# Optimization experiments

Hardware: AMD Instinct MI355X
Metric: run time of the kernel (lower is better)

The kernel has to match this reference:

```python
import jax, jax.numpy as jnp
import numpy as np

EMB_DIM = 1024
N_HEAD = 16
HEAD_SIZE = 64
B = 2
T = 2048


def setup_inputs() -> dict:
    key = jax.random.key(0)
    k_x, k_qkv, k_pw, k_pb = jax.random.split(key, 4)
    x = jax.random.normal(k_x, (B, T, EMB_DIM), dtype=jnp.float32)
    # nn.Linear(emb_dim, 3*emb_dim, bias=False): y = x @ W_qkv, W_qkv: [C, 3C]
    W_qkv = jax.random.normal(k_qkv, (EMB_DIM, 3 * EMB_DIM), dtype=jnp.float32) * (EMB_DIM ** -0.5)
    # nn.Linear(emb_dim, emb_dim) with bias
    W_proj = jax.random.normal(k_pw, (EMB_DIM, EMB_DIM), dtype=jnp.float32) * (EMB_DIM ** -0.5)
    b_proj = jax.random.normal(k_pb, (EMB_DIM,), dtype=jnp.float32) * 0.01
    return {"x": x, "W_qkv": W_qkv, "W_proj": W_proj, "b_proj": b_proj}


def reference(x, W_qkv, W_proj, b_proj):
    Bn, Tn, C = x.shape
    qkv = x @ W_qkv                          # [B, T, 3C]
    q, k, v = jnp.split(qkv, 3, axis=-1)
    # [B, T, H, D] -> attention over heads via einsum (no explicit transpose)
    q = q.reshape(Bn, Tn, N_HEAD, HEAD_SIZE)
    k = k.reshape(Bn, Tn, N_HEAD, HEAD_SIZE)
    v = v.reshape(Bn, Tn, N_HEAD, HEAD_SIZE)
    att = jnp.einsum("bthd,bshd->bhts", q, k) * (HEAD_SIZE ** -0.5)  # [B, H, T, T]
    causal = jnp.tril(jnp.ones((Tn, Tn), dtype=bool))
    att = jnp.where(causal, att, -jnp.inf)
    att = jax.nn.softmax(att, axis=-1)
    y = jnp.einsum("bhts,bshd->bthd", att, v).reshape(Bn, Tn, C)
    return y @ W_proj + b_proj
```

## Files before the change

kernel.cpp:

```cpp
#include <hip/hip_runtime.h>
#include <hip/hip_bf16.h>

typedef unsigned short u16;
typedef unsigned int u32;
typedef u16 u16x4 __attribute__((ext_vector_type(4)));
typedef u16 u16x8 __attribute__((ext_vector_type(8)));
typedef u32 u32x4 __attribute__((ext_vector_type(4)));
typedef __bf16 bf16x8 __attribute__((ext_vector_type(8)));
typedef float f32x4 __attribute__((ext_vector_type(4)));

__device__ __forceinline__ u16 f2bf(float f) {
  union { float f; unsigned u; } v; v.f = f;
  unsigned r = v.u + 0x7fffu + ((v.u >> 16) & 1u);
  return (u16)(r >> 16);
}

__device__ __forceinline__ u16 bf(float f) {
  __bf16 h = (__bf16)f;
  union { __bf16 h; u16 u; } c; c.h = h;
  return c.u;
}

__device__ __forceinline__ u32 pack2(float lo, float hi) {
  return (u32)bf(lo) | ((u32)bf(hi) << 16);
}

__device__ __forceinline__ float fexp2(float x) {
#if __has_builtin(__builtin_amdgcn_exp2f)
  return __builtin_amdgcn_exp2f(x);
#else
  return exp2f(x);
#endif
}

__device__ __forceinline__ float frcp(float x) {
#if __has_builtin(__builtin_amdgcn_rcpf)
  return __builtin_amdgcn_rcpf(x);
#else
  return 1.0f / x;
#endif
}

__device__ __forceinline__ void gload16(const void* g, void* l) {
  __builtin_amdgcn_global_load_lds((const __attribute__((address_space(1))) void*)g,
                                   (__attribute__((address_space(3))) void*)l, 16, 0, 0);
}

__global__ __launch_bounds__(256) void cvt_bf16(const float* __restrict__ in,
                                                u16* __restrict__ out, int n) {
  int i = (blockIdx.x * 256 + threadIdx.x) * 8;
  if (i >= n) return;
  f32x4 a = *(const f32x4*)(in + i);
  f32x4 b = *(const f32x4*)(in + i + 4);
  u16x8 r;
  r[0] = f2bf(a[0]); r[1] = f2bf(a[1]); r[2] = f2bf(a[2]); r[3] = f2bf(a[3]);
  r[4] = f2bf(b[0]); r[5] = f2bf(b[1]); r[6] = f2bf(b[2]); r[7] = f2bf(b[3]);
  *(u16x8*)(out + i) = r;
}

__global__ __launch_bounds__(256) void transpose_w(
    const float* __restrict__ Wqkv, const float* __restrict__ Wproj,
    u16* __restrict__ wqT, u16* __restrict__ wpT)
{
  __shared__ float tile[32][33];
  int bx = blockIdx.x;
  const float* in;
  u16* out;
  int N;
  if (bx < 96) { in = Wqkv; out = wqT; N = 3072; }
  else         { in = Wproj; out = wpT; N = 1024; bx -= 96; }
  const int K = 1024;
  int n0 = bx * 32, k0 = blockIdx.y * 32;
  int tx = threadIdx.x & 31, ty = threadIdx.x >> 5;
  for (int i = 0; i < 32; i += 8)
    tile[ty + i][tx] = in[(long)(k0 + ty + i) * N + n0 + tx];
  __syncthreads();
  for (int i = 0; i < 32; i += 8)
    out[(long)(n0 + ty + i) * K + k0 + tx] = f2bf(tile[tx][ty + i]);
}

template<int BM, int BN, bool F32OUT>
__global__ __launch_bounds__(256) void gemm_bt(
    const u16* __restrict__ A, const u16* __restrict__ Bt,
    void* __restrict__ Cp, const float* __restrict__ bias,
    int M, int N, int K)
{
  constexpr int MR = BM / 32, NR = BN / 32;
  constexpr int RA = BM / 32, RB = BN / 32;
  __shared__ char lds[(BM + BN) * 128];
  char* As = lds;
  char* Bs = lds + BM * 128;
  const int tid = threadIdx.x;
  const int l = tid & 63, w = tid >> 6;
  const int wr = w >> 1, wc = w & 1;
  const int lr = l & 15, q4 = l >> 4;
  const long row0 = (long)blockIdx.x * BM;
  const long col0 = (long)blockIdx.y * BN;

  f32x4 acc[MR][NR] = {};

  const u16* gA[RA];
  int oA[RA];
  for (int i = 0; i < RA; ++i) {
    int cc = i * 256 + tid;
    int r = cc >> 3, c = (cc & 7) ^ (r & 7);
    oA[i] = cc * 16;
    gA[i] = A + (row0 + r) * K + c * 8;
  }
  const u16* gB[RB];
  int oB[RB];
  for (int i = 0; i < RB; ++i) {
    int cc = i * 256 + tid;
    int r = cc >> 3, c = (cc & 7) ^ (r & 7);
    oB[i] = cc * 16;
    gB[i] = Bt + (col0 + r) * K + c * 8;
  }

  for (int k0 = 0; k0 < K; k0 += 64) {
    __syncthreads();
    for (int i = 0; i < RA; ++i) gload16(gA[i] + k0, As + oA[i]);
    for (int i = 0; i < RB; ++i) gload16(gB[i] + k0, Bs + oB[i]);
    __syncthreads();
    for (int kk = 0; kk < 2; ++kk) {
      bf16x8 a[MR], b[NR];
      for (int m = 0; m < MR; ++m) {
        int r = wr * (BM / 2) + m * 16 + lr;
        a[m] = *(const bf16x8*)(As + r * 128 + (((kk * 4 + q4) ^ (r & 7)) << 4));
      }
      for (int n = 0; n < NR; ++n) {
        int r = wc * (BN / 2) + n * 16 + lr;
        b[n] = *(const bf16x8*)(Bs + r * 128 + (((kk * 4 + q4) ^ (r & 7)) << 4));
      }
      for (int m = 0; m < MR; ++m)
        for (int n = 0; n < NR; ++n)
          acc[m][n] = __builtin_amdgcn_mfma_f32_16x16x32_bf16(a[m], b[n], acc[m][n], 0, 0, 0);
    }
  }

  for (int n = 0; n < NR; ++n) {
    int col = (int)col0 + wc * (BN / 2) + n * 16 + lr;
    float bv = 0.f;
    if (F32OUT) bv = bias[col];
    for (int m = 0; m < MR; ++m) {
      for (int reg = 0; reg < 4; ++reg) {
        long row = row0 + wr * (BM / 2) + m * 16 + q4 * 4 + reg;
        float vv = acc[m][n][reg] + bv;
        if (F32OUT) ((float*)Cp)[row * N + col] = vv;
        else        ((u16*)Cp)[row * N + col] = f2bf(vv);
      }
    }
  }
}

#define FXOR(d) (((((d) & 7) ^ (((d) >> 3) & 7))) << 4)

#define VSCAT(vtb, ra, rb)                                                     \
  for (int j = 0; j < 4; ++j) {                                                \
    int d = vd0 + j;                                                           \
    *(u32*)((vtb) + d * 128 + (vcol2 ^ FXOR(d))) = (u32)(ra)[j] | ((u32)(rb)[j] << 16); \
  }

#define COMPUTE_TILE(T)                                                        \
  if (64 * (T) <= wrow + 15) {                                                 \
    char* ks_ = ksmem + ((T) & 3) * 8192;                                      \
    char* vt_ = vtmem + ((T) & 3) * 8192;                                      \
    const int k0_ = 64 * (T);                                                  \
    f32x4 st[4] = {};                                                          \
    __builtin_amdgcn_s_setprio(1);                                             \
    for (int kk = 0; kk < 2; ++kk)                                             \
      for (int n = 0; n < 4; ++n) {                                            \
        int r = n * 16 + lr;                                                   \
        int c = (kk * 4 + g) ^ (r & 7);                                        \
        bf16x8 kf = *(const bf16x8*)(ks_ + r * 128 + (c << 4));                \
        st[n] = __builtin_amdgcn_mfma_f32_16x16x32_bf16(kf, qf[kk], st[n], 0, 0, 0); \
      }                                                                        \
    __builtin_amdgcn_s_setprio(0);                                             \
    if (k0_ + 63 > wrow) {                                                     \
      for (int n = 0; n < 4; ++n)                                              \
        for (int reg = 0; reg < 4; ++reg)                                      \
          if (k0_ + n * 16 + g * 4 + reg > wrow + lr)                          \
            st[n][reg] = -__builtin_inff();                                    \
    }                                                                          \
    float psum = 0.f;                                                          \
    u32 pk[4][2];                                                              \
    for (int n = 0; n < 4; ++n) {                                              \
      float p0 = fexp2(st[n][0]), p1 = fexp2(st[n][1]);                        \
      float p2 = fexp2(st[n][2]), p3 = fexp2(st[n][3]);                        \
      psum += (p0 + p1) + (p2 + p3);                                           \
      pk[n][0] = pack2(p0, p1);                                                \
      pk[n][1] = pack2(p2, p3);                                                \
    }                                                                          \
    lsum += psum;                                                              \
    __builtin_amdgcn_s_setprio(1);                                             \
    for (int kt = 0; kt < 2; ++kt) {                                           \
      u32x4 pb;                                                                \
      pb[0] = pk[2 * kt][0]; pb[1] = pk[2 * kt][1];                            \
      pb[2] = pk[2 * kt + 1][0]; pb[3] = pk[2 * kt + 1][1];                    \
      bf16x8 pf = *(bf16x8*)&pb;                                               \
      for (int n = 0; n < 4; ++n) {                                            \
        int dd = n * 16 + lr;                                                  \
        bf16x8 vf = *(const bf16x8*)(vt_ + dd * 128 + ((kt * 64 + g * 16) ^ FXOR(dd))); \
        o[n] = __builtin_amdgcn_mfma_f32_16x16x32_bf16(vf, pf, o[n], 0, 0, 0); \
      }                                                                        \
    }                                                                          \
    __builtin_amdgcn_s_setprio(0);                                             \
  }

__global__ __launch_bounds__(512) void attn_fwd(
    const u16* __restrict__ qkv, u16* __restrict__ atty)
{
  __shared__ char ksmem[4 * 8192];
  __shared__ char vtmem[4 * 8192];
  const int tid = threadIdx.x;
  const int l = tid & 63, w = tid >> 6;
  const int lr = l & 15, g = l >> 4;
  const int h = blockIdx.y;
  const int ti = blockIdx.x;
  const long base = (long)blockIdx.z * 2048;
  const int wrow = (w < 4) ? (ti * 64 + w * 16) : ((31 - ti) * 64 + (w - 4) * 16);

  bf16x8 qf[2];
  for (int kk = 0; kk < 2; ++kk) {
    u16x8 raw = *(const u16x8*)(qkv + (base + wrow + lr) * 3072 + h * 64 + kk * 32 + g * 8);
    u16x8 sc;
    for (int j = 0; j < 8; ++j) {
      union { unsigned u; float f; } c; c.u = ((unsigned)raw[j]) << 16;
      sc[j] = bf(c.f * 0.18033688f);
    }
    qf[kk] = *(bf16x8*)&sc;
  }

  float lsum = 0.f;
  f32x4 o[4] = {};

  const int kr = tid >> 3, kc = (tid & 7) ^ (kr & 7);
  const u16* kg = qkv + (base + kr) * 3072 + 1024 + h * 64 + kc * 8;
  const int va = tid >> 4;
  const int vd0 = (tid & 15) * 4;
  const int vk0 = va * 2;
  const int vn = vk0 >> 4, vgp2 = (vk0 >> 2) & 3, vr = vk0 & 3;
  const int vcol2 = ((vn >> 1) * 32 + vgp2 * 8 + (vn & 1) * 4 + vr) * 2;
  const u16* vgp = qkv + (base + vk0) * 3072 + 2048 + h * 64 + vd0;

  const int nkv = 32 - ti;

  {
    u16x4 a0 = *(const u16x4*)(vgp);
    u16x4 b0 = *(const u16x4*)(vgp + 3072);
    u16x4 a1 = *(const u16x4*)(vgp + 196608);
    u16x4 b1 = *(const u16x4*)(vgp + 196608 + 3072);
    gload16(kg, ksmem + tid * 16);
    gload16(kg + 196608, ksmem + 8192 + tid * 16);
    VSCAT(vtmem, a0, b0);
    VSCAT(vtmem + 8192, a1, b1);
  }
  __syncthreads();

  for (int tb = 0; tb < nkv; tb += 2) {
    u16x4 p2a, p2b, p3a, p3b;
    const bool pf2 = (tb + 2) < nkv, pf3 = (tb + 3) < nkv;
    if (pf2) {
      long off = (long)(tb + 2) * 196608;
      p2a = *(const u16x4*)(vgp + off);
      p2b = *(const u16x4*)(vgp + off + 3072);
      gload16(kg + off, ksmem + ((tb + 2) & 3) * 8192 + tid * 16);
    }
    if (pf3) {
      long off = (long)(tb + 3) * 196608;
      p3a = *(const u16x4*)(vgp + off);
      p3b = *(const u16x4*)(vgp + off + 3072);
      gload16(kg + off, ksmem + ((tb + 3) & 3) * 8192 + tid * 16);
    }

    COMPUTE_TILE(tb);
    if (tb + 1 < nkv) COMPUTE_TILE(tb + 1);

    if (pf2) VSCAT(vtmem + ((tb + 2) & 3) * 8192, p2a, p2b);
    if (pf3) VSCAT(vtmem + ((tb + 3) & 3) * 8192, p3a, p3b);
    __syncthreads();
  }

  lsum += __shfl_xor(lsum, 16);
  lsum += __shfl_xor(lsum, 32);
  float inv = frcp(lsum);
  long row = base + wrow + lr;
  for (int n = 0; n < 4; ++n) {
    u16x4 ov;
    for (int reg = 0; reg < 4; ++reg) ov[reg] = bf(o[n][reg] * inv);
    *(u16x4*)(atty + row * 1024 + h * 64 + n * 16 + g * 4) = ov;
  }
}

extern "C" void kernel_launch(void* const* d_in, const int* in_sizes, int n_in,
                              void* d_out, int out_size, void* d_ws, size_t ws_size,
                              hipStream_t stream) {
  const float* x     = (const float*)d_in[0];
  const float* Wqkv  = (const float*)d_in[1];
  const float* Wproj = (const float*)d_in[2];
  const float* bproj = (const float*)d_in[3];
  char* ws = (char*)d_ws;
  u16* xb   = (u16*)(ws);
  u16* wqT  = (u16*)(ws + 8388608);
  u16* wpT  = (u16*)(ws + 14680064);
  u16* qkv  = (u16*)(ws + 16777216);
  u16* atty = (u16*)(ws + 41943040);

  cvt_bf16<<<2048, 256, 0, stream>>>(x, xb, 4194304);
  transpose_w<<<dim3(128, 32), 256, 0, stream>>>(Wqkv, Wproj, wqT, wpT);
  gemm_bt<128, 128, false><<<dim3(32, 24), 256, 0, stream>>>(xb, wqT, (void*)qkv, nullptr, 4096, 3072, 1024);
  attn_fwd<<<dim3(16, 16, 2), 512, 0, stream>>>(qkv, atty);
  gemm_bt<128, 64, true><<<dim3(32, 16), 256, 0, stream>>>(atty, wpT, d_out, bproj, 4096, 1024, 1024);
}
```

Measured before the change: 107.6 us.

## Interleave QK/softmax/PV across two KV tiles, fuse prep kernels, reorder blocks

The attention inner loop now issues the QK MFMAs for both KV tiles first, then both softmax steps, then both PV steps. This gives the scheduler independent MFMA and exp work to overlap, at the cost of more live registers. The fp32->bf16 conversion of x and the weight transpose are merged into one launch to save a kernel launch. For batch 1, the block-to-tile mapping is reversed to spread causal work unevenly across dispatch order.

```diff
diff --git a/kernel.cpp b/kernel.cpp
--- a/kernel.cpp
+++ b/kernel.cpp
@@ -46,31 +46,32 @@
                                    (__attribute__((address_space(3))) void*)l, 16, 0, 0);
 }
 
-__global__ __launch_bounds__(256) void cvt_bf16(const float* __restrict__ in,
-                                                u16* __restrict__ out, int n) {
-  int i = (blockIdx.x * 256 + threadIdx.x) * 8;
-  if (i >= n) return;
-  f32x4 a = *(const f32x4*)(in + i);
-  f32x4 b = *(const f32x4*)(in + i + 4);
-  u16x8 r;
-  r[0] = f2bf(a[0]); r[1] = f2bf(a[1]); r[2] = f2bf(a[2]); r[3] = f2bf(a[3]);
-  r[4] = f2bf(b[0]); r[5] = f2bf(b[1]); r[6] = f2bf(b[2]); r[7] = f2bf(b[3]);
-  *(u16x8*)(out + i) = r;
-}
-
-__global__ __launch_bounds__(256) void transpose_w(
-    const float* __restrict__ Wqkv, const float* __restrict__ Wproj,
+__global__ __launch_bounds__(256) void prep(
+    const float* __restrict__ x, const float* __restrict__ Wqkv,
+    const float* __restrict__ Wproj, u16* __restrict__ xb,
     u16* __restrict__ wqT, u16* __restrict__ wpT)
 {
   __shared__ float tile[32][33];
-  int bx = blockIdx.x;
+  const int bid = blockIdx.x;
+  if (bid < 2048) {
+    int i = (bid * 256 + threadIdx.x) * 8;
+    f32x4 a = *(const f32x4*)(x + i);
+    f32x4 b = *(const f32x4*)(x + i + 4);
+    u16x8 r;
+    r[0] = f2bf(a[0]); r[1] = f2bf(a[1]); r[2] = f2bf(a[2]); r[3] = f2bf(a[3]);
+    r[4] = f2bf(b[0]); r[5] = f2bf(b[1]); r[6] = f2bf(b[2]); r[7] = f2bf(b[3]);
+    *(u16x8*)(xb + i) = r;
+    return;
+  }
+  int flat = bid - 2048;
+  int bx = flat & 127, by = flat >> 7;
   const float* in;
   u16* out;
   int N;
   if (bx < 96) { in = Wqkv; out = wqT; N = 3072; }
   else         { in = Wproj; out = wpT; N = 1024; bx -= 96; }
   const int K = 1024;
-  int n0 = bx * 32, k0 = blockIdx.y * 32;
+  int n0 = bx * 32, k0 = by * 32;
   int tx = threadIdx.x & 31, ty = threadIdx.x >> 5;
   for (int i = 0; i < 32; i += 8)
     tile[ty + i][tx] = in[(long)(k0 + ty + i) * N + n0 + tx];
@@ -160,42 +161,45 @@
     *(u32*)((vtb) + d * 128 + (vcol2 ^ FXOR(d))) = (u32)(ra)[j] | ((u32)(rb)[j] << 16); \
   }
 
-#define COMPUTE_TILE(T)                                                        \
-  if (64 * (T) <= wrow + 15) {                                                 \
+#define QK_TILE(T, ST)                                                         \
+  {                                                                            \
     char* ks_ = ksmem + ((T) & 3) * 8192;                                      \
-    char* vt_ = vtmem + ((T) & 3) * 8192;                                      \
-    const int k0_ = 64 * (T);                                                  \
-    f32x4 st[4] = {};                                                          \
-    __builtin_amdgcn_s_setprio(1);                                             \
     for (int kk = 0; kk < 2; ++kk)                                             \
       for (int n = 0; n < 4; ++n) {                                            \
         int r = n * 16 + lr;                                                   \
         int c = (kk * 4 + g) ^ (r & 7);                                        \
         bf16x8 kf = *(const bf16x8*)(ks_ + r * 128 + (c << 4));                \
-        st[n] = __builtin_amdgcn_mfma_f32_16x16x32_bf16(kf, qf[kk], st[n], 0, 0, 0); \
+        ST[n] = __builtin_amdgcn_mfma_f32_16x16x32_bf16(kf, qf[kk], ST[n], 0, 0, 0); \
       }                                                                        \
-    __builtin_amdgcn_s_setprio(0);                                             \
+  }
+
+#define SM_TILE(T, ST, PK)                                                     \
+  {                                                                            \
+    const int k0_ = 64 * (T);                                                  \
     if (k0_ + 63 > wrow) {                                                     \
       for (int n = 0; n < 4; ++n)                                              \
         for (int reg = 0; reg < 4; ++reg)                                      \
           if (k0_ + n * 16 + g * 4 + reg > wrow + lr)                          \
-            st[n][reg] = -__builtin_inff();                                    \
+            ST[n][reg] = -__builtin_inff();                                    \
     }                                                                          \
     float psum = 0.f;                                                          \
-    u32 pk[4][2];                                                              \
     for (int n = 0; n < 4; ++n) {                                              \
-      float p0 = fexp2(st[n][0]), p1 = fexp2(st[n][1]);                        \
-      float p2 = fexp2(st[n][2]), p3 = fexp2(st[n][3]);                        \
+      float p0 = fexp2(ST[n][0]), p1 = fexp2(ST[n][1]);                        \
+      float p2 = fexp2(ST[n][2]), p3 = fexp2(ST[n][3]);                        \
       psum += (p0 + p1) + (p2 + p3);                                           \
-      pk[n][0] = pack2(p0, p1);                                                \
-      pk[n][1] = pack2(p2, p3);                                                \
+      PK[n][0] = pack2(p0, p1);                                                \
+      PK[n][1] = pack2(p2, p3);                                                \
     }                                                                          \
     lsum += psum;                                                              \
-    __builtin_amdgcn_s_setprio(1);                                             \
+  }
+
+#define PV_TILE(T, PK)                                                         \
+  {                                                                            \
+    char* vt_ = vtmem + ((T) & 3) * 8192;                                      \
     for (int kt = 0; kt < 2; ++kt) {                                           \
       u32x4 pb;                                                                \
-      pb[0] = pk[2 * kt][0]; pb[1] = pk[2 * kt][1];                            \
-      pb[2] = pk[2 * kt + 1][0]; pb[3] = pk[2 * kt + 1][1];                    \
+      pb[0] = PK[2 * kt][0]; pb[1] = PK[2 * kt][1];                            \
+      pb[2] = PK[2 * kt + 1][0]; pb[3] = PK[2 * kt + 1][1];                    \
       bf16x8 pf = *(bf16x8*)&pb;                                               \
       for (int n = 0; n < 4; ++n) {                                            \
         int dd = n * 16 + lr;                                                  \
@@ -203,7 +207,6 @@
         o[n] = __builtin_amdgcn_mfma_f32_16x16x32_bf16(vf, pf, o[n], 0, 0, 0); \
       }                                                                        \
     }                                                                          \
-    __builtin_amdgcn_s_setprio(0);                                             \
   }
 
 __global__ __launch_bounds__(512) void attn_fwd(
@@ -215,7 +218,7 @@
   const int l = tid & 63, w = tid >> 6;
   const int lr = l & 15, g = l >> 4;
   const int h = blockIdx.y;
-  const int ti = blockIdx.x;
+  const int ti = blockIdx.z ? (15 - (int)blockIdx.x) : (int)blockIdx.x;
   const long base = (long)blockIdx.z * 2048;
   const int wrow = (w < 4) ? (ti * 64 + w * 16) : ((31 - ti) * 64 + (w - 4) * 16);
 
@@ -272,8 +275,22 @@
       gload16(kg + off, ksmem + ((tb + 3) & 3) * 8192 + tid * 16);
     }
 
-    COMPUTE_TILE(tb);
-    if (tb + 1 < nkv) COMPUTE_TILE(tb + 1);
+    {
+      const bool a0 = 64 * tb <= wrow + 15;
+      const bool a1 = (tb + 1 < nkv) && (64 * (tb + 1) <= wrow + 15);
+      f32x4 st0[4] = {}, st1[4] = {};
+      u32 pk0[4][2], pk1[4][2];
+      __builtin_amdgcn_s_setprio(1);
+      if (a0) QK_TILE(tb, st0);
+      if (a1) QK_TILE(tb + 1, st1);
+      __builtin_amdgcn_s_setprio(0);
+      if (a0) SM_TILE(tb, st0, pk0);
+      if (a1) SM_TILE(tb + 1, st1, pk1);
+      __builtin_amdgcn_s_setprio(1);
+      if (a0) PV_TILE(tb, pk0);
+      if (a1) PV_TILE(tb + 1, pk1);
+      __builtin_amdgcn_s_setprio(0);
+    }
 
     if (pf2) VSCAT(vtmem + ((tb + 2) & 3) * 8192, p2a, p2b);
     if (pf3) VSCAT(vtmem + ((tb + 3) & 3) * 8192, p3a, p3b);
@@ -305,8 +322,7 @@
   u16* qkv  = (u16*)(ws + 16777216);
   u16* atty = (u16*)(ws + 41943040);
 
-  cvt_bf16<<<2048, 256, 0, stream>>>(x, xb, 4194304);
-  transpose_w<<<dim3(128, 32), 256, 0, stream>>>(Wqkv, Wproj, wqT, wpT);
+  prep<<<6144, 256, 0, stream>>>(x, Wqkv, Wproj, xb, wqT, wpT);
   gemm_bt<128, 128, false><<<dim3(32, 24), 256, 0, stream>>>(xb, wqT, (void*)qkv, nullptr, 4096, 3072, 1024);
   attn_fwd<<<dim3(16, 16, 2), 512, 0, stream>>>(qkv, atty);
   gemm_bt<128, 64, true><<<dim3(32, 16), 256, 0, stream>>>(atty, wpT, d_out, bproj, 4096, 1024, 1024);
```

Measured after the change: 123.8 us. 15.0% more time.
